# Kernel optimization log

Hardware: AMD Instinct MI355X
Metric: run time of the kernel (lower is better)

The kernel has to match this reference:

```python
import jax, jax.numpy as jnp
import numpy as np

TOPK = 300
NUM_LEVELS = 3
GATE_TEMP = 1.0


def _normalized_grid(h, w):
    # matches torch: linspace(-1,1) meshgrid 'ij', stack (xx, yy) -> [h*w, 2]
    y = jnp.linspace(-1.0, 1.0, h, dtype=jnp.float32)
    x = jnp.linspace(-1.0, 1.0, w, dtype=jnp.float32)
    yy, xx = jnp.meshgrid(y, x, indexing='ij')
    return jnp.stack((xx, yy), axis=-1).reshape(h * w, 2)


def setup_inputs() -> dict:
    key = jax.random.key(0)
    ks = jax.random.split(key, 10)
    C, H_DIM, MAXL = 256, 256, 8
    shapes = [(8, C, 100, 152), (8, C, 50, 76), (8, C, 25, 38)]
    inp = {}
    for i, s in enumerate(shapes):
        inp[f'f{i}'] = jax.random.normal(ks[i], s, dtype=jnp.float32)
    inp['conv_w'] = jax.random.normal(ks[3], (C,), dtype=jnp.float32) * (1.0 / np.sqrt(C))
    inp['conv_b'] = jnp.zeros((1,), dtype=jnp.float32)
    inp['level_emb'] = jax.random.normal(ks[4], (MAXL, H_DIM), dtype=jnp.float32)
    qin = C + H_DIM + 3  # 515
    inp['w1'] = jax.random.normal(ks[5], (qin, H_DIM), dtype=jnp.float32) * (1.0 / np.sqrt(qin))
    inp['b1'] = jnp.zeros((H_DIM,), dtype=jnp.float32)
    inp['w2'] = jax.random.normal(ks[6], (H_DIM, H_DIM), dtype=jnp.float32) * (1.0 / np.sqrt(H_DIM))
    inp['b2'] = jnp.zeros((H_DIM,), dtype=jnp.float32)
    inp['gate_w'] = jax.random.normal(ks[7], (H_DIM, MAXL), dtype=jnp.float32) * (1.0 / np.sqrt(H_DIM))
    inp['gate_b'] = jnp.zeros((MAXL,), dtype=jnp.float32)
    inp['residual_scale'] = jnp.zeros((1,), dtype=jnp.float32)  # residual_scale_init=0.0
    return inp


def reference(f0, f1, f2, conv_w, conv_b, level_emb, w1, b1, w2, b2, gate_w, gate_b, residual_scale):
    levels = [f0, f1, f2]
    B = f0.shape[0]
    tok_s, tok_f, tok_p, tok_l = [], [], [], []
    for i, f in enumerate(levels):
        _, C, H, W = f.shape
        # 1x1 conv proxy objectness score -> [B, H*W]
        s = jnp.einsum('bchw,c->bhw', f, conv_w).reshape(B, H * W) + conv_b[0]
        tok_s.append(s)
        tok_f.append(f.reshape(B, C, H * W).transpose(0, 2, 1))       # [B, HW, C]
        tok_p.append(jnp.broadcast_to(_normalized_grid(H, W), (B, H * W, 2)))
        tok_l.append(jnp.full((B, H * W), i, dtype=jnp.int32))
    scores = jnp.concatenate(tok_s, axis=1)   # [B, N]
    feats = jnp.concatenate(tok_f, axis=1)    # [B, N, C]
    pos = jnp.concatenate(tok_p, axis=1)      # [B, N, 2]
    lvl = jnp.concatenate(tok_l, axis=1)      # [B, N]

    top_vals, top_idx = jax.lax.top_k(scores, TOPK)                     # [B, K]
    fk = jnp.take_along_axis(feats, top_idx[:, :, None], axis=1)        # [B, K, C]
    pk = jnp.take_along_axis(pos, top_idx[:, :, None], axis=1)          # [B, K, 2]
    lk = jnp.take_along_axis(lvl, top_idx, axis=1)                      # [B, K]
    sp = jax.nn.sigmoid(top_vals)                                       # [B, K]

    q = jnp.concatenate([fk, level_emb[lk], pk, sp[..., None]], axis=-1)  # [B, K, C+H+3]
    h = jax.nn.relu(q @ w1 + b1)
    h = jax.nn.relu(h @ w2 + b2)
    logits = (h @ gate_w + gate_b)[..., :NUM_LEVELS]                     # [B, K, L]
    gates = jax.nn.softmax(logits / GATE_TEMP, axis=-1)
    alpha = gates.mean(axis=1)                                           # [B, L]
    scale = 1.0 + residual_scale[0] * alpha                              # [B, L]

    outs = [f * scale[:, i][:, None, None, None] for i, f in enumerate(levels)]
    # flatten the output feature dict into one [B, sum(C*H*W)] array
    return jnp.concatenate([o.reshape(B, -1) for o in outs], axis=1)
```

## Files before the change

### kernel.cpp

```cpp
#include <hip/hip_runtime.h>
#include <hip/hip_bf16.h>

#define NTOK 19950
#define NTOKP 19968
#define KTOP 300
#define NB 8
#define NQ 2400
#define QDIM 520
#define NCC 16
#define CAND 4096

typedef float f32x4 __attribute__((ext_vector_type(4)));

__device__ __forceinline__ uint32_t fkey(float f) {
    uint32_t u = __float_as_uint(f);
    return (u & 0x80000000u) ? ~u : (u | 0x80000000u);
}

__device__ __forceinline__ void suffix_scan_256(int* hist, int tid) {
    if (tid < 64) {
        const int c0 = hist[tid * 4], c1 = hist[tid * 4 + 1];
        const int c2 = hist[tid * 4 + 2], c3 = hist[tid * 4 + 3];
        const int tot = c0 + c1 + c2 + c3;
        int s = tot;
        #pragma unroll
        for (int off = 1; off < 64; off <<= 1) {
            int o = __shfl_down(s, off);
            if (tid + off < 64) s += o;
        }
        const int Sn = s - tot;
        hist[tid * 4 + 3] = c3 + Sn;
        hist[tid * 4 + 2] = c2 + c3 + Sn;
        hist[tid * 4 + 1] = c1 + c2 + c3 + Sn;
        hist[tid * 4 + 0] = tot + Sn;
    }
}

__global__ __launch_bounds__(256) void score_part_kernel(
    const float* __restrict__ f0, const float* __restrict__ f1, const float* __restrict__ f2,
    const float* __restrict__ conv_w, float* __restrict__ partial, int* __restrict__ ghist)
{
    __shared__ float cwch[16];
    const int tid = threadIdx.x;
    const int blk = blockIdx.x;
    int b, cc;
    if (blk < 512)      { b = blk >> 6; cc = (blk >> 2) & 15; }
    else if (blk < 640) { int i = blk - 512; b = i >> 4; cc = i & 15; }
    else                { int i = blk - 640; b = i >> 4; cc = i & 15; }
    if (blk >= 640 && ((blk - 640) & 15) == 0 && tid < 256)
        ghist[((blk - 640) >> 4) * 256 + tid] = 0;
    if (tid < 16) cwch[tid] = conv_w[cc * 16 + tid];
    __syncthreads();

    if (blk < 512) {
        const int q = blk & 3;
        const f32x4* b4 = (const f32x4*)(f0 + ((size_t)(b * 256 + cc * 16)) * 15200) + q * 950;
        const int s3 = (tid + 768 < 950) ? tid + 768 : 0;
        f32x4 a0 = {0,0,0,0}, a1 = a0, a2 = a0, a3 = a0;
        #pragma unroll 4
        for (int c = 0; c < 16; ++c) {
            const f32x4* r = b4 + (size_t)c * 3800;
            const float w = cwch[c];
            f32x4 v0 = r[tid], v1 = r[tid + 256], v2 = r[tid + 512], v3 = r[s3];
            a0 += v0 * w; a1 += v1 * w; a2 += v2 * w; a3 += v3 * w;
        }
        f32x4* o4 = (f32x4*)(partial + (size_t)(cc * NB + b) * NTOKP) + q * 950;
        o4[tid] = a0; o4[tid + 256] = a1; o4[tid + 512] = a2;
        if (tid + 768 < 950) o4[tid + 768] = a3;
    } else if (blk < 640) {
        const f32x4* b4 = (const f32x4*)(f1 + ((size_t)(b * 256 + cc * 16)) * 3800);
        const int s3 = (tid + 768 < 950) ? tid + 768 : 0;
        f32x4 a0 = {0,0,0,0}, a1 = a0, a2 = a0, a3 = a0;
        #pragma unroll 4
        for (int c = 0; c < 16; ++c) {
            const f32x4* r = b4 + (size_t)c * 950;
            const float w = cwch[c];
            f32x4 v0 = r[tid], v1 = r[tid + 256], v2 = r[tid + 512], v3 = r[s3];
            a0 += v0 * w; a1 += v1 * w; a2 += v2 * w; a3 += v3 * w;
        }
        f32x4* o4 = (f32x4*)(partial + (size_t)(cc * NB + b) * NTOKP + 15200);
        o4[tid] = a0; o4[tid + 256] = a1; o4[tid + 512] = a2;
        if (tid + 768 < 950) o4[tid + 768] = a3;
    } else {
        const float2* b2 = (const float2*)(f2 + ((size_t)(b * 256 + cc * 16)) * 950);
        const int s1 = (tid + 256 < 475) ? tid + 256 : 0;
        float2 a0 = {0,0}, a1 = a0;
        #pragma unroll 4
        for (int c = 0; c < 16; ++c) {
            const float2* r = b2 + (size_t)c * 475;
            const float w = cwch[c];
            float2 v0 = r[tid], v1 = r[s1];
            a0.x += v0.x * w; a0.y += v0.y * w;
            a1.x += v1.x * w; a1.y += v1.y * w;
        }
        float2* o2 = (float2*)(partial + (size_t)(cc * NB + b) * NTOKP + 19000);
        if (tid < 475) o2[tid] = a0;
        if (tid + 256 < 475) o2[tid + 256] = a1;
    }
}

__global__ __launch_bounds__(256) void score_reduce_kernel(
    const float* __restrict__ partial, const float* __restrict__ conv_b,
    float* __restrict__ scores, int* __restrict__ ghist)
{
    __shared__ int lh[256];
    const int tid = threadIdx.x;
    const int b = blockIdx.y;
    const int i = blockIdx.x * 256 + tid;
    lh[tid] = 0;
    __syncthreads();
    if (i < NTOK) {
        float s = 0.0f;
        #pragma unroll
        for (int cc = 0; cc < NCC; ++cc)
            s += partial[(size_t)(cc * NB + b) * NTOKP + i];
        s += conv_b[0];
        scores[b * NTOK + i] = s;
        atomicAdd(&lh[fkey(s) >> 24], 1);
    }
    __syncthreads();
    if (lh[tid]) atomicAdd(&ghist[b * 256 + tid], lh[tid]);
}

__global__ __launch_bounds__(1024, 1) void topk_kernel(
    const float* __restrict__ scores, const int* __restrict__ ghist,
    int* __restrict__ top_idx)
{
    __shared__ int hist[257];
    __shared__ uint32_t ck[CAND];
    __shared__ int ci[CAND];
    __shared__ int tie[1024];
    __shared__ uint32_t s_prefix;
    __shared__ int s_Kr, s_cnt, s_ccnt, s_tcnt;
    const int tid = threadIdx.x;
    const int b = blockIdx.x;
    const float* srow = scores + b * NTOK;

    if (tid < 256) hist[tid] = ghist[b * 256 + tid];
    if (tid == 0) { hist[256] = 0; s_cnt = 0; s_ccnt = 0; s_tcnt = 0; }
    __syncthreads();
    suffix_scan_256(hist, tid);
    __syncthreads();
    if (tid < 256) {
        int sgeq = hist[tid], sgt = hist[tid + 1];
        if (sgeq >= KTOP && sgt < KTOP) {
            s_prefix = (uint32_t)tid << 24;
            s_Kr = KTOP - sgt;
        }
    }
    __syncthreads();
    const uint32_t v = s_prefix >> 24;

    for (int i = tid; i < NTOK; i += 1024) {
        uint32_t k = fkey(srow[i]);
        uint32_t tb = k >> 24;
        if (tb > v) {
            int p = atomicAdd(&s_cnt, 1);
            top_idx[b * KTOP + p] = i;
        } else if (tb == v) {
            int p = atomicAdd(&s_ccnt, 1);
            if (p < CAND) { ck[p] = k; ci[p] = i; }
        }
    }
    __syncthreads();
    const int ccnt = s_ccnt;
    const int ncand = ccnt < CAND ? ccnt : CAND;
    const bool fits = (ccnt <= CAND);

    uint32_t pmask = 0xFF000000u;
    for (int pass = 1; pass < 4; ++pass) {
        const int shift = 24 - 8 * pass;
        if (tid < 257) hist[tid] = 0;
        __syncthreads();
        const uint32_t prefix = s_prefix;
        const int Kr = s_Kr;
        if (fits) {
            for (int j = tid; j < ncand; j += 1024) {
                uint32_t k = ck[j];
                if ((k & pmask) == prefix) atomicAdd(&hist[(k >> shift) & 255], 1);
            }
        } else {
            for (int i = tid; i < NTOK; i += 1024) {
                uint32_t k = fkey(srow[i]);
                if ((k & pmask) == prefix) atomicAdd(&hist[(k >> shift) & 255], 1);
            }
        }
        __syncthreads();
        suffix_scan_256(hist, tid);
        __syncthreads();
        if (tid < 256) {
            int sgeq = hist[tid], sgt = hist[tid + 1];
            if (sgeq >= Kr && sgt < Kr) {
                s_prefix = prefix | ((uint32_t)tid << shift);
                s_Kr = Kr - sgt;
            }
        }
        __syncthreads();
        pmask |= (0xFFu << shift);
    }
    const uint32_t T = s_prefix;
    const int need = s_Kr;

    if (fits) {
        for (int j = tid; j < ncand; j += 1024) {
            uint32_t k = ck[j];
            if (k > T) {
                int p = atomicAdd(&s_cnt, 1);
                top_idx[b * KTOP + p] = ci[j];
            } else if (k == T) {
                int p = atomicAdd(&s_tcnt, 1);
                if (p < 1024) tie[p] = ci[j];
            }
        }
    } else {
        for (int i = tid; i < NTOK; i += 1024) {
            uint32_t k = fkey(srow[i]);
            if ((k >> 24) == v) {
                if (k > T) {
                    int p = atomicAdd(&s_cnt, 1);
                    top_idx[b * KTOP + p] = i;
                } else if (k == T) {
                    int p = atomicAdd(&s_tcnt, 1);
                    if (p < 1024) tie[p] = i;
                }
            }
        }
    }
    __syncthreads();
    if (tid == 0) {
        int base = s_cnt;
        int tcnt = s_tcnt > 1024 ? 1024 : s_tcnt;
        for (int s = 0; s < need; ++s) {
            int mi = s;
            for (int u = s + 1; u < tcnt; ++u) if (tie[u] < tie[mi]) mi = u;
            int tmp = tie[s]; tie[s] = tie[mi]; tie[mi] = tmp;
            top_idx[b * KTOP + base + s] = tie[s];
        }
    }
}

#define QT 8
__global__ __launch_bounds__(512, 1) void mlp_kernel(
    const float* __restrict__ f0, const float* __restrict__ f1, const float* __restrict__ f2,
    const float* __restrict__ scores, const int* __restrict__ top_idx,
    const float* __restrict__ level_emb,
    const float* __restrict__ w1, const float* __restrict__ b1,
    const float* __restrict__ w2, const float* __restrict__ b2,
    const float* __restrict__ gate_w, const float* __restrict__ gate_b,
    float* __restrict__ G)
{
    __shared__ __align__(16) float q[QT][QDIM];
    __shared__ __align__(16) float part[QT][256];
    __shared__ __align__(16) float h[QT][256];
    __shared__ int s_b[QT], s_lvl[QT], s_hw[QT], s_HW[QT];
    const int tid = threadIdx.x;
    const int out = tid & 255;
    const int kh = tid >> 8;
    const int k0 = blockIdx.x * QT;

    if (tid < QT) {
        const int kk = k0 + tid;
        const int bq = kk / KTOP;
        const int idx = top_idx[kk];
        int lvl, hw, HWl, Wl, Hl;
        if (idx < 15200)      { lvl = 0; hw = idx;         HWl = 15200; Wl = 152; Hl = 100; }
        else if (idx < 19000) { lvl = 1; hw = idx - 15200; HWl = 3800;  Wl = 76;  Hl = 50;  }
        else                  { lvl = 2; hw = idx - 19000; HWl = 950;   Wl = 38;  Hl = 25;  }
        s_b[tid] = bq; s_lvl[tid] = lvl; s_hw[tid] = hw; s_HW[tid] = HWl;
        int hh = hw / Wl, ww = hw - hh * Wl;
        float x = -1.0f + 2.0f * (float)ww / (float)(Wl - 1);
        float y = -1.0f + 2.0f * (float)hh / (float)(Hl - 1);
        float sv = scores[bq * NTOK + idx];
        float sp = 1.0f / (1.0f + expf(-sv));
        q[tid][512] = x; q[tid][513] = y; q[tid][514] = sp;
        q[tid][515] = 0.0f; q[tid][516] = 0.0f; q[tid][517] = 0.0f;
        q[tid][518] = 0.0f; q[tid][519] = 0.0f;
    }
    __syncthreads();
    #pragma unroll
    for (int j = tid; j < QT * 256; j += 512) {
        const int t = j >> 8, c = j & 255;
        const int lvl = s_lvl[t];
        const float* f = (lvl == 0) ? f0 : ((lvl == 1) ? f1 : f2);
        q[t][c]       = f[((size_t)(s_b[t] * 256 + c)) * s_HW[t] + s_hw[t]];
        q[t][256 + c] = level_emb[lvl * 256 + c];
    }
    __syncthreads();

    float acc[QT];

    {
        #pragma unroll
        for (int t = 0; t < QT; ++t) acc[t] = 0.0f;
        const float* wp = w1 + (size_t)(kh * 256) * 256 + out;
        float a0 = wp[0], a1 = wp[256], a2 = wp[512], a3 = wp[768];
        for (int i4 = 0; i4 < 64; ++i4) {
            float c0 = a0, c1 = a1, c2 = a2, c3 = a3;
            const float* wn = wp + 1024;
            if (i4 < 63) { a0 = wn[0]; a1 = wn[256]; a2 = wn[512]; a3 = wn[768]; }
            wp = wn;
            const int kb = kh * 256 + i4 * 4;
            #pragma unroll
            for (int t = 0; t < QT; ++t) {
                float4 qv = *reinterpret_cast<const float4*>(&q[t][kb]);
                acc[t] += qv.x * c0 + qv.y * c1 + qv.z * c2 + qv.w * c3;
            }
        }
        if (kh) {
            for (int r = 512; r < 515; ++r) {
                float wv = w1[(size_t)r * 256 + out];
                #pragma unroll
                for (int t = 0; t < QT; ++t) acc[t] += q[t][r] * wv;
            }
            #pragma unroll
            for (int t = 0; t < QT; ++t) part[t][out] = acc[t];
        }
    }
    __syncthreads();
    if (kh == 0) {
        float bj = b1[out];
        #pragma unroll
        for (int t = 0; t < QT; ++t) h[t][out] = fmaxf(acc[t] + part[t][out] + bj, 0.0f);
    }
    __syncthreads();

    {
        #pragma unroll
        for (int t = 0; t < QT; ++t) acc[t] = 0.0f;
        const float* wp = w2 + (size_t)(kh * 128) * 256 + out;
        float a0 = wp[0], a1 = wp[256], a2 = wp[512], a3 = wp[768];
        for (int i4 = 0; i4 < 32; ++i4) {
            float c0 = a0, c1 = a1, c2 = a2, c3 = a3;
            const float* wn = wp + 1024;
            if (i4 < 31) { a0 = wn[0]; a1 = wn[256]; a2 = wn[512]; a3 = wn[768]; }
            wp = wn;
            const int kb = kh * 128 + i4 * 4;
            #pragma unroll
            for (int t = 0; t < QT; ++t) {
                float4 hv = *reinterpret_cast<const float4*>(&h[t][kb]);
                acc[t] += hv.x * c0 + hv.y * c1 + hv.z * c2 + hv.w * c3;
            }
        }
        if (kh) {
            #pragma unroll
            for (int t = 0; t < QT; ++t) part[t][out] = acc[t];
        }
    }
    __syncthreads();
    if (kh == 0) {
        float bj = b2[out];
        #pragma unroll
        for (int t = 0; t < QT; ++t) q[t][out] = fmaxf(acc[t] + part[t][out] + bj, 0.0f);
    }
    __syncthreads();

    if (tid < 256) {
        const int t = tid >> 5, seg = tid & 31;
        float l0 = 0.f, l1 = 0.f, l2 = 0.f;
        for (int c = seg * 8; c < seg * 8 + 8; ++c) {
            float hv = q[t][c];
            l0 += hv * gate_w[c * 8 + 0];
            l1 += hv * gate_w[c * 8 + 1];
            l2 += hv * gate_w[c * 8 + 2];
        }
        float* gp = &part[0][0];
        gp[(t * 32 + seg) * 3 + 0] = l0;
        gp[(t * 32 + seg) * 3 + 1] = l1;
        gp[(t * 32 + seg) * 3 + 2] = l2;
    }
    __syncthreads();
    if (tid < QT) {
        const int t = tid;
        float l0 = gate_b[0], l1 = gate_b[1], l2 = gate_b[2];
        const float* gp = &part[0][0];
        for (int seg = 0; seg < 32; ++seg) {
            l0 += gp[(t * 32 + seg) * 3 + 0];
            l1 += gp[(t * 32 + seg) * 3 + 1];
            l2 += gp[(t * 32 + seg) * 3 + 2];
        }
        float m = fmaxf(l0, fmaxf(l1, l2));
        float e0 = expf(l0 - m), e1 = expf(l1 - m), e2 = expf(l2 - m);
        float inv = 1.0f / (e0 + e1 + e2);
        G[(k0 + t) * 3 + 0] = e0 * inv;
        G[(k0 + t) * 3 + 1] = e1 * inv;
        G[(k0 + t) * 3 + 2] = e2 * inv;
    }
}

__global__ __launch_bounds__(256) void out_kernel(
    const f32x4* __restrict__ f0, const f32x4* __restrict__ f1, const f32x4* __restrict__ f2,
    const float* __restrict__ G, const float* __restrict__ rs, f32x4* __restrict__ out)
{
    __shared__ float red[3][32];
    __shared__ float ssc[3];
    const int b = blockIdx.y;
    const int tid = threadIdx.x;
    if (tid < 96) {
        const int l = tid / 32, c = tid % 32;
        float s = 0.0f;
        const int kb = c * 10;
        const int ke = (kb + 10 < KTOP) ? kb + 10 : KTOP;
        for (int k = kb; k < ke; ++k) s += G[(size_t)(b * KTOP + k) * 3 + l];
        red[l][c] = s;
    }
    __syncthreads();
    for (int off = 16; off > 0; off >>= 1) {
        if (tid < 96) {
            const int l = tid / 32, c = tid % 32;
            if (c < off) red[l][c] += red[l][c + off];
        }
        __syncthreads();
    }
    if (tid < 3) ssc[tid] = 1.0f + rs[0] * (red[tid][0] / (float)KTOP);
    __syncthreads();

    const int t0 = blockIdx.x * 256 + tid;
    const int TPB = gridDim.x * 256;
    f32x4* ob = out + (size_t)b * 1276800;
    {
        const float sc = ssc[0];
        const f32x4* src = f0 + (size_t)b * 972800;
        for (int r = t0; r < 972800; r += TPB)
            __builtin_nontemporal_store(src[r] * sc, &ob[r]);
    }
    {
        const float sc = ssc[1];
        const f32x4* src = f1 + (size_t)b * 243200;
        f32x4* o1 = ob + 972800;
        for (int r = t0; r < 243200; r += TPB)
            __builtin_nontemporal_store(src[r] * sc, &o1[r]);
    }
    {
        const float sc = ssc[2];
        const f32x4* src = f2 + (size_t)b * 60800;
        f32x4* o2 = ob + 1216000;
        for (int r = t0; r < 60800; r += TPB)
            __builtin_nontemporal_store(src[r] * sc, &o2[r]);
    }
}

extern "C" void kernel_launch(void* const* d_in, const int* in_sizes, int n_in,
                              void* d_out, int out_size, void* d_ws, size_t ws_size,
                              hipStream_t stream)
{
    const float* f0        = (const float*)d_in[0];
    const float* f1        = (const float*)d_in[1];
    const float* f2        = (const float*)d_in[2];
    const float* conv_w    = (const float*)d_in[3];
    const float* conv_b    = (const float*)d_in[4];
    const float* level_emb = (const float*)d_in[5];
    const float* w1        = (const float*)d_in[6];
    const float* b1        = (const float*)d_in[7];
    const float* w2        = (const float*)d_in[8];
    const float* b2        = (const float*)d_in[9];
    const float* gate_w    = (const float*)d_in[10];
    const float* gate_b    = (const float*)d_in[11];
    const float* rs        = (const float*)d_in[12];

    char* ws = (char*)d_ws;
    float* scores  = (float*)ws;
    int*   top_idx = (int*)(ws + 640 * 1024);
    float* G       = (float*)(ws + 656 * 1024);
    int*   ghist   = (int*)(ws + 688 * 1024);
    float* partial = (float*)(ws + 704 * 1024);

    score_part_kernel<<<768, 256, 0, stream>>>(f0, f1, f2, conv_w, partial, ghist);
    score_reduce_kernel<<<dim3(78, NB), 256, 0, stream>>>(partial, conv_b, scores, ghist);
    topk_kernel<<<NB, 1024, 0, stream>>>(scores, ghist, top_idx);
    mlp_kernel<<<NQ / QT, 512, 0, stream>>>(f0, f1, f2, scores, top_idx, level_emb,
                                            w1, b1, w2, b2, gate_w, gate_b, G);
    out_kernel<<<dim3(512, NB), 256, 0, stream>>>((const f32x4*)f0, (const f32x4*)f1,
                                                  (const f32x4*)f2, G, rs, (f32x4*)d_out);
}
```

Before: 164.8 us.

## Split top-k into grid-wide emit pass and per-batch refine; tile output copy per block

The single-block-per-batch top-k kernel is split into a grid-wide emit kernel that scans all scores in parallel and writes candidates for the threshold bucket to global memory. A small refine kernel then loads those candidates and finishes the radix passes with 256 threads. Separately, the output scaling kernel now gives each block a contiguous chunk of each level instead of a grid-stride loop, with half as many blocks. This adds one kernel launch and global atomics on per-batch counters.

```diff
diff --git a/kernel.cpp b/kernel.cpp
--- a/kernel.cpp
+++ b/kernel.cpp
@@ -38,7 +38,8 @@
 
 __global__ __launch_bounds__(256) void score_part_kernel(
     const float* __restrict__ f0, const float* __restrict__ f1, const float* __restrict__ f2,
-    const float* __restrict__ conv_w, float* __restrict__ partial, int* __restrict__ ghist)
+    const float* __restrict__ conv_w, float* __restrict__ partial, int* __restrict__ ghist,
+    int* __restrict__ cnt)
 {
     __shared__ float cwch[16];
     const int tid = threadIdx.x;
@@ -49,6 +50,7 @@
     else                { int i = blk - 640; b = i >> 4; cc = i & 15; }
     if (blk >= 640 && ((blk - 640) & 15) == 0 && tid < 256)
         ghist[((blk - 640) >> 4) * 256 + tid] = 0;
+    if (blk == 640 && tid < 16) cnt[tid] = 0;
     if (tid < 16) cwch[tid] = conv_w[cc * 16 + tid];
     __syncthreads();
 
@@ -122,78 +124,95 @@
     if (lh[tid]) atomicAdd(&ghist[b * 256 + tid], lh[tid]);
 }
 
-__global__ __launch_bounds__(1024, 1) void topk_kernel(
+__global__ __launch_bounds__(256) void topk_emit_kernel(
     const float* __restrict__ scores, const int* __restrict__ ghist,
-    int* __restrict__ top_idx)
+    int* __restrict__ cnt, int* __restrict__ top_idx,
+    uint32_t* __restrict__ cand_k, int* __restrict__ cand_i)
+{
+    __shared__ int sfx[257];
+    __shared__ int s_v;
+    const int tid = threadIdx.x;
+    const int b = blockIdx.y;
+    const int i = blockIdx.x * 256 + tid;
+    sfx[tid] = ghist[b * 256 + tid];
+    if (tid == 0) sfx[256] = 0;
+    __syncthreads();
+    suffix_scan_256(sfx, tid);
+    __syncthreads();
+    if (sfx[tid] >= KTOP && sfx[tid + 1] < KTOP) s_v = tid;
+    __syncthreads();
+    const uint32_t v = (uint32_t)s_v;
+    if (i < NTOK) {
+        uint32_t k = fkey(scores[b * NTOK + i]);
+        uint32_t tb = k >> 24;
+        if (tb > v) {
+            int p = atomicAdd(&cnt[b], 1);
+            top_idx[b * KTOP + p] = i;
+        } else if (tb == v) {
+            int p = atomicAdd(&cnt[8 + b], 1);
+            if (p < CAND) { cand_k[b * CAND + p] = k; cand_i[b * CAND + p] = i; }
+        }
+    }
+}
+
+__global__ __launch_bounds__(256, 1) void topk_refine_kernel(
+    const float* __restrict__ scores, const int* __restrict__ ghist,
+    const int* __restrict__ cnt, int* __restrict__ top_idx,
+    const uint32_t* __restrict__ cand_k, const int* __restrict__ cand_i)
 {
     __shared__ int hist[257];
     __shared__ uint32_t ck[CAND];
     __shared__ int ci[CAND];
     __shared__ int tie[1024];
     __shared__ uint32_t s_prefix;
-    __shared__ int s_Kr, s_cnt, s_ccnt, s_tcnt;
+    __shared__ int s_Kr, s_cnt, s_tcnt;
     const int tid = threadIdx.x;
     const int b = blockIdx.x;
-    const float* srow = scores + b * NTOK;
-
-    if (tid < 256) hist[tid] = ghist[b * 256 + tid];
-    if (tid == 0) { hist[256] = 0; s_cnt = 0; s_ccnt = 0; s_tcnt = 0; }
+
+    hist[tid] = ghist[b * 256 + tid];
+    if (tid == 0) { hist[256] = 0; s_tcnt = 0; }
     __syncthreads();
     suffix_scan_256(hist, tid);
     __syncthreads();
-    if (tid < 256) {
-        int sgeq = hist[tid], sgt = hist[tid + 1];
-        if (sgeq >= KTOP && sgt < KTOP) {
-            s_prefix = (uint32_t)tid << 24;
-            s_Kr = KTOP - sgt;
-        }
+    if (hist[tid] >= KTOP && hist[tid + 1] < KTOP) {
+        s_prefix = (uint32_t)tid << 24;
+        s_Kr = KTOP - hist[tid + 1];
+        s_cnt = hist[tid + 1];
     }
     __syncthreads();
     const uint32_t v = s_prefix >> 24;
-
-    for (int i = tid; i < NTOK; i += 1024) {
-        uint32_t k = fkey(srow[i]);
-        uint32_t tb = k >> 24;
-        if (tb > v) {
-            int p = atomicAdd(&s_cnt, 1);
-            top_idx[b * KTOP + p] = i;
-        } else if (tb == v) {
-            int p = atomicAdd(&s_ccnt, 1);
-            if (p < CAND) { ck[p] = k; ci[p] = i; }
-        }
-    }
-    __syncthreads();
-    const int ccnt = s_ccnt;
-    const int ncand = ccnt < CAND ? ccnt : CAND;
+    const int ccnt = cnt[8 + b];
     const bool fits = (ccnt <= CAND);
+    const int ncand = fits ? ccnt : CAND;
+    if (fits)
+        for (int j = tid; j < ncand; j += 256) { ck[j] = cand_k[b * CAND + j]; ci[j] = cand_i[b * CAND + j]; }
+    __syncthreads();
 
     uint32_t pmask = 0xFF000000u;
     for (int pass = 1; pass < 4; ++pass) {
         const int shift = 24 - 8 * pass;
-        if (tid < 257) hist[tid] = 0;
+        hist[tid] = 0;
+        if (tid == 0) hist[256] = 0;
         __syncthreads();
         const uint32_t prefix = s_prefix;
         const int Kr = s_Kr;
         if (fits) {
-            for (int j = tid; j < ncand; j += 1024) {
+            for (int j = tid; j < ncand; j += 256) {
                 uint32_t k = ck[j];
                 if ((k & pmask) == prefix) atomicAdd(&hist[(k >> shift) & 255], 1);
             }
         } else {
-            for (int i = tid; i < NTOK; i += 1024) {
-                uint32_t k = fkey(srow[i]);
+            for (int i = tid; i < NTOK; i += 256) {
+                uint32_t k = fkey(scores[b * NTOK + i]);
                 if ((k & pmask) == prefix) atomicAdd(&hist[(k >> shift) & 255], 1);
             }
         }
         __syncthreads();
         suffix_scan_256(hist, tid);
         __syncthreads();
-        if (tid < 256) {
-            int sgeq = hist[tid], sgt = hist[tid + 1];
-            if (sgeq >= Kr && sgt < Kr) {
-                s_prefix = prefix | ((uint32_t)tid << shift);
-                s_Kr = Kr - sgt;
-            }
+        if (hist[tid] >= Kr && hist[tid + 1] < Kr) {
+            s_prefix = prefix | ((uint32_t)tid << shift);
+            s_Kr = Kr - hist[tid + 1];
         }
         __syncthreads();
         pmask |= (0xFFu << shift);
@@ -202,7 +221,7 @@
     const int need = s_Kr;
 
     if (fits) {
-        for (int j = tid; j < ncand; j += 1024) {
+        for (int j = tid; j < ncand; j += 256) {
             uint32_t k = ck[j];
             if (k > T) {
                 int p = atomicAdd(&s_cnt, 1);
@@ -213,8 +232,8 @@
             }
         }
     } else {
-        for (int i = tid; i < NTOK; i += 1024) {
-            uint32_t k = fkey(srow[i]);
+        for (int i = tid; i < NTOK; i += 256) {
+            uint32_t k = fkey(scores[b * NTOK + i]);
             if ((k >> 24) == v) {
                 if (k > T) {
                     int p = atomicAdd(&s_cnt, 1);
@@ -228,7 +247,7 @@
     }
     __syncthreads();
     if (tid == 0) {
-        int base = s_cnt;
+        const int base = KTOP - need;
         int tcnt = s_tcnt > 1024 ? 1024 : s_tcnt;
         for (int s = 0; s < need; ++s) {
             int mi = s;
@@ -414,28 +433,33 @@
     if (tid < 3) ssc[tid] = 1.0f + rs[0] * (red[tid][0] / (float)KTOP);
     __syncthreads();
 
-    const int t0 = blockIdx.x * 256 + tid;
-    const int TPB = gridDim.x * 256;
+    const int bx = blockIdx.x;
     f32x4* ob = out + (size_t)b * 1276800;
     {
         const float sc = ssc[0];
-        const f32x4* src = f0 + (size_t)b * 972800;
-        for (int r = t0; r < 972800; r += TPB)
-            __builtin_nontemporal_store(src[r] * sc, &ob[r]);
+        const f32x4* src = f0 + (size_t)b * 972800 + bx * 3800;
+        f32x4* dst = ob + bx * 3800;
+        #pragma unroll 4
+        for (int r = tid; r < 3800; r += 256)
+            __builtin_nontemporal_store(src[r] * sc, &dst[r]);
     }
     {
         const float sc = ssc[1];
-        const f32x4* src = f1 + (size_t)b * 243200;
-        f32x4* o1 = ob + 972800;
-        for (int r = t0; r < 243200; r += TPB)
-            __builtin_nontemporal_store(src[r] * sc, &o1[r]);
+        const f32x4* src = f1 + (size_t)b * 243200 + bx * 950;
+        f32x4* dst = ob + 972800 + bx * 950;
+        #pragma unroll 4
+        for (int r = tid; r < 950; r += 256)
+            __builtin_nontemporal_store(src[r] * sc, &dst[r]);
     }
     {
         const float sc = ssc[2];
-        const f32x4* src = f2 + (size_t)b * 60800;
-        f32x4* o2 = ob + 1216000;
-        for (int r = t0; r < 60800; r += TPB)
-            __builtin_nontemporal_store(src[r] * sc, &o2[r]);
+        const int base = bx * 238;
+        const int lim = (base + 238 < 60800) ? 238 : (60800 - base);
+        const f32x4* src = f2 + (size_t)b * 60800 + base;
+        f32x4* dst = ob + 1216000 + base;
+        #pragma unroll 2
+        for (int r = tid; r < lim; r += 256)
+            __builtin_nontemporal_store(src[r] * sc, &dst[r]);
     }
 }
 
@@ -458,17 +482,21 @@
     const float* rs        = (const float*)d_in[12];
 
     char* ws = (char*)d_ws;
-    float* scores  = (float*)ws;
-    int*   top_idx = (int*)(ws + 640 * 1024);
-    float* G       = (float*)(ws + 656 * 1024);
-    int*   ghist   = (int*)(ws + 688 * 1024);
-    float* partial = (float*)(ws + 704 * 1024);
-
-    score_part_kernel<<<768, 256, 0, stream>>>(f0, f1, f2, conv_w, partial, ghist);
+    float*    scores  = (float*)ws;
+    int*      top_idx = (int*)(ws + 640 * 1024);
+    float*    G       = (float*)(ws + 656 * 1024);
+    int*      ghist   = (int*)(ws + 688 * 1024);
+    int*      cnt     = (int*)(ws + 696 * 1024);
+    uint32_t* cand_k  = (uint32_t*)(ws + 704 * 1024);
+    int*      cand_i  = (int*)(ws + 832 * 1024);
+    float*    partial = (float*)(ws + 1024 * 1024);
+
+    score_part_kernel<<<768, 256, 0, stream>>>(f0, f1, f2, conv_w, partial, ghist, cnt);
     score_reduce_kernel<<<dim3(78, NB), 256, 0, stream>>>(partial, conv_b, scores, ghist);
-    topk_kernel<<<NB, 1024, 0, stream>>>(scores, ghist, top_idx);
+    topk_emit_kernel<<<dim3(78, NB), 256, 0, stream>>>(scores, ghist, cnt, top_idx, cand_k, cand_i);
+    topk_refine_kernel<<<NB, 256, 0, stream>>>(scores, ghist, cnt, top_idx, cand_k, cand_i);
     mlp_kernel<<<NQ / QT, 512, 0, stream>>>(f0, f1, f2, scores, top_idx, level_emb,
                                             w1, b1, w2, b2, gate_w, gate_b, G);
-    out_kernel<<<dim3(512, NB), 256, 0, stream>>>((const f32x4*)f0, (const f32x4*)f1,
+    out_kernel<<<dim3(256, NB), 256, 0, stream>>>((const f32x4*)f0, (const f32x4*)f1,
                                                   (const f32x4*)f2, G, rs, (f32x4*)d_out);
 }
```

Result: slower. 234.8 us (+42.5%).
